# Performance work log

Hardware: AMD Instinct MI355X
Metric: run time of the kernel (lower is better)

## Reference

```python
import jax, jax.numpy as jnp
import numpy as np

DIAG = 64          # dynamic_mask_scale: |i-j| >= DIAG is masked
NEG_INF = float('-inf')

def _band_mask(L, diagonal):
    # True where masked out: j >= i + diagonal or i >= j + diagonal  <=>  |i-j| >= diagonal
    i = jnp.arange(L)[:, None]
    j = jnp.arange(L)[None, :]
    return jnp.abs(i - j) >= diagonal  # [L, L] bool

def setup_inputs() -> dict:
    key = jax.random.key(0)
    k1, k2, k3, k4 = jax.random.split(key, 4)
    B, L, H, E = 2, 2048, 8, 64
    queries = jax.random.normal(k1, (B, L, H, E), dtype=jnp.float32)
    keys = jax.random.normal(k2, (B, L, H, E), dtype=jnp.float32)
    values = jax.random.normal(k3, (B, L, H, E), dtype=jnp.float32)
    sigma = jax.random.normal(k4, (B, L, H), dtype=jnp.float32)
    attn_mask = jnp.zeros((B, 1, L, L), dtype=bool)  # unused (dynamic mask path)
    return {"queries": queries, "keys": keys, "values": values,
            "sigma": sigma, "attn_mask": attn_mask}

def reference(queries, keys, values, sigma, attn_mask):
    B, L, H, E = queries.shape
    scale = 1.0 / jnp.sqrt(jnp.float32(E))
    # scores: [B, H, L, S]
    scores = jnp.einsum('blhe,bshe->bhls', queries, keys)
    mask = _band_mask(L, DIAG)  # [L, L]
    scores = jnp.where(mask[None, None, :, :], NEG_INF, scores)
    attn = scale * scores
    series = jax.nn.softmax(attn, axis=-1)  # dropout p=0 -> identity
    V = jnp.einsum('bhls,bshd->blhd', series, values)
    return (V, series)
```

## Files before the change

### kernel.cpp

```cpp
#include <hip/hip_runtime.h>
#include <cstdint>

#define BB    2
#define LL    2048
#define HH    8
#define EE    64
#define DIAG  64
#define RR    16
#define WCAP  144
#define SK    68
#define PS    160
#define NT    256

__global__ __launch_bounds__(NT, 3) void anomaly_attn_kernel(
    const float* __restrict__ Q,
    const float* __restrict__ K,
    const float* __restrict__ V,
    float* __restrict__ outV,
    float* __restrict__ outS)
{
    __shared__ float lds_kv[WCAP * SK];
    __shared__ float lds_q[RR * EE];
    __shared__ float lds_sp[RR * PS];

    const int bid  = blockIdx.x;
    const int gblk = (bid & 7) * 256 + (bid >> 3);
    const int rb   = gblk & 127;
    const int h    = (gblk >> 7) & 7;
    const int b    = gblk >> 10;
    const int i0   = rb * RR;

    const int t    = threadIdx.x;
    const int wave = t >> 6;
    const int lane = t & 63;

    const size_t headOff = ((size_t)b * LL * HH + h) * EE;
    const int    rowStr  = HH * EE;

    const int j0 = i0 - (DIAG - 1);

    {
        const float4 z4 = make_float4(0.f, 0.f, 0.f, 0.f);
        float4* zp = (float4*)(lds_sp + wave * 4 * PS);
        for (int z = lane; z < 160; z += 64) zp[z] = z4;
    }

    {
        const int qrow = t >> 4, qf = t & 15;
        *(float4*)(lds_q + qrow * EE + qf * 4) =
            *(const float4*)(Q + headOff + (size_t)(i0 + qrow) * rowStr + qf * 4);
        for (int idx = t; idx < WCAP * 16; idx += NT) {
            const int trow = idx >> 4, tf = idx & 15;
            int j = j0 + trow; j = j < 0 ? 0 : (j > LL - 1 ? LL - 1 : j);
            *(float4*)(lds_kv + trow * SK + tf * 4) =
                *(const float4*)(K + headOff + (size_t)j * rowStr + tf * 4);
        }
    }
    __syncthreads();

    const float scale = 0.125f;
    for (int r4 = 0; r4 < 4; ++r4) {
        const int r = wave * 4 + r4;
        const int i = i0 + r;
        const float* qrow = lds_q + r * EE;
        const float* k1   = lds_kv + (r + lane) * SK;
        const float* k2   = k1 + 64 * SK;
        float s1 = 0.f, s2 = 0.f;
#pragma unroll
        for (int c = 0; c < 16; ++c) {
            const float4 q4 = *(const float4*)(qrow + c * 4);
            const float4 a4 = *(const float4*)(k1 + c * 4);
            const float4 b4 = *(const float4*)(k2 + c * 4);
            s1 += q4.x * a4.x + q4.y * a4.y + q4.z * a4.z + q4.w * a4.w;
            s2 += q4.x * b4.x + q4.y * b4.y + q4.z * b4.z + q4.w * b4.w;
        }
        const int  slot2 = lane + 64;
        const bool v1 = (i - (DIAG - 1) + lane) >= 0;
        const bool v2 = (slot2 < 2 * DIAG - 1) && (i - (DIAG - 1) + slot2 < LL);
        float sc1 = v1 ? s1 * scale : -3.0e38f;
        float sc2 = v2 ? s2 * scale : -3.0e38f;

        float m = fmaxf(sc1, sc2);
#pragma unroll
        for (int off = 1; off < 64; off <<= 1)
            m = fmaxf(m, __shfl_xor(m, off, 64));
        float p1 = v1 ? __expf(sc1 - m) : 0.f;
        float p2 = v2 ? __expf(sc2 - m) : 0.f;
        float l = p1 + p2;
#pragma unroll
        for (int off = 1; off < 64; off <<= 1)
            l += __shfl_xor(l, off, 64);
        const float inv = 1.0f / l;
        float* prow = lds_sp + r * PS;
        prow[16 + lane]      = p1 * inv;
        prow[80 + lane]      = p2 * inv;
    }
    __syncthreads();

    for (int idx = t; idx < WCAP * 16; idx += NT) {
        const int trow = idx >> 4, tf = idx & 15;
        int j = j0 + trow; j = j < 0 ? 0 : (j > LL - 1 ? LL - 1 : j);
        *(float4*)(lds_kv + trow * SK + tf * 4) =
            *(const float4*)(V + headOff + (size_t)j * rowStr + tf * 4);
    }
    __syncthreads();

    for (int r4 = 0; r4 < 4; ++r4) {
        const int r = wave * 4 + r4;
        const int i = i0 + r;
        float4* srow4 = (float4*)(outS + (((size_t)(b * HH + h)) * LL + i) * LL);
        const int start = i - (DIAG - 1);
        const float* sp = lds_sp + r * PS + 16;
#pragma unroll
        for (int k = 0; k < 8; ++k) {
            const int col4 = lane + k * 64;
            const int d0   = col4 * 4 - start;
            float4 v;
            int i0c = d0     < 0 ? 0 : (d0     > 127 ? 127 : d0);
            int i1c = d0 + 1 < 0 ? 0 : (d0 + 1 > 127 ? 127 : d0 + 1);
            int i2c = d0 + 2 < 0 ? 0 : (d0 + 2 > 127 ? 127 : d0 + 2);
            int i3c = d0 + 3 < 0 ? 0 : (d0 + 3 > 127 ? 127 : d0 + 3);
            v.x = (d0     >= 0) ? sp[i0c] : 0.f;
            v.y = (d0 + 1 >= 0) ? sp[i1c] : 0.f;
            v.z = (d0 + 2 >= 0) ? sp[i2c] : 0.f;
            v.w = (d0 + 3 >= 0) ? sp[i3c] : 0.f;
            srow4[col4] = v;
        }
    }

    {
        const int e4   = lane & 15;
        const int jsub = lane >> 4;
        const int rr0  = wave * 4;
        const float* pbase = lds_sp + rr0 * (PS - 1) + 16;
        float4 a0 = make_float4(0,0,0,0), a1 = a0, a2 = a0, a3 = a0;
#pragma unroll
        for (int k = 0; k < WCAP / 4; ++k) {
            const int jrel = jsub + 4 * k;
            const float4 vv = *(const float4*)(lds_kv + jrel * SK + e4 * 4);
            const float w0 = pbase[jrel];
            const float w1 = pbase[(PS - 1) + jrel];
            const float w2 = pbase[2 * (PS - 1) + jrel];
            const float w3 = pbase[3 * (PS - 1) + jrel];
            a0.x += w0 * vv.x; a0.y += w0 * vv.y; a0.z += w0 * vv.z; a0.w += w0 * vv.w;
            a1.x += w1 * vv.x; a1.y += w1 * vv.y; a1.z += w1 * vv.z; a1.w += w1 * vv.w;
            a2.x += w2 * vv.x; a2.y += w2 * vv.y; a2.z += w2 * vv.z; a2.w += w2 * vv.w;
            a3.x += w3 * vv.x; a3.y += w3 * vv.y; a3.z += w3 * vv.z; a3.w += w3 * vv.w;
        }
#pragma unroll
        for (int off = 16; off <= 32; off <<= 1) {
            a0.x += __shfl_xor(a0.x, off, 64); a0.y += __shfl_xor(a0.y, off, 64);
            a0.z += __shfl_xor(a0.z, off, 64); a0.w += __shfl_xor(a0.w, off, 64);
            a1.x += __shfl_xor(a1.x, off, 64); a1.y += __shfl_xor(a1.y, off, 64);
            a1.z += __shfl_xor(a1.z, off, 64); a1.w += __shfl_xor(a1.w, off, 64);
            a2.x += __shfl_xor(a2.x, off, 64); a2.y += __shfl_xor(a2.y, off, 64);
            a2.z += __shfl_xor(a2.z, off, 64); a2.w += __shfl_xor(a2.w, off, 64);
            a3.x += __shfl_xor(a3.x, off, 64); a3.y += __shfl_xor(a3.y, off, 64);
            a3.z += __shfl_xor(a3.z, off, 64); a3.w += __shfl_xor(a3.w, off, 64);
        }
        if (lane < 16) {
            float4* o0 = (float4*)(outV + headOff + (size_t)(i0 + rr0 + 0) * rowStr);
            float4* o1 = (float4*)(outV + headOff + (size_t)(i0 + rr0 + 1) * rowStr);
            float4* o2 = (float4*)(outV + headOff + (size_t)(i0 + rr0 + 2) * rowStr);
            float4* o3 = (float4*)(outV + headOff + (size_t)(i0 + rr0 + 3) * rowStr);
            o0[e4] = a0; o1[e4] = a1; o2[e4] = a2; o3[e4] = a3;
        }
    }
}

extern "C" void kernel_launch(void* const* d_in, const int* in_sizes, int n_in,
                              void* d_out, int out_size, void* d_ws, size_t ws_size,
                              hipStream_t stream) {
    const float* Q = (const float*)d_in[0];
    const float* K = (const float*)d_in[1];
    const float* V = (const float*)d_in[2];

    float* outV = (float*)d_out;
    float* outS = (float*)d_out + (size_t)BB * LL * HH * EE;

    const int grid = (BB * HH * LL) / RR;
    anomaly_attn_kernel<<<grid, NT, 0, stream>>>(Q, K, V, outV, outS);
}
```

Baseline: 344.2 us.

## Store probabilities in aligned window layout and pair rows in score computation

Switches the probability scratch layout from per-row diagonal offsets to a shared 4-aligned window starting at i0-64, so each score row can be written to global memory with aligned float4 LDS reads instead of four clamped scalar gathers. The QK score loop now processes two rows per iteration, sharing each K load between both rows. The reductions for the two rows are interleaved. The PV loop uses a plain stride. The kernel is dominated by the dense [L,L] score-matrix write, so the gain is mostly in instruction overhead around that store.

```diff
diff --git a/kernel.cpp b/kernel.cpp
--- a/kernel.cpp
+++ b/kernel.cpp
@@ -9,7 +9,7 @@
 #define RR    16
 #define WCAP  144
 #define SK    68
-#define PS    160
+#define PS    148
 #define NT    256
 
 __global__ __launch_bounds__(NT, 3) void anomaly_attn_kernel(
@@ -37,12 +37,13 @@
     const size_t headOff = ((size_t)b * LL * HH + h) * EE;
     const int    rowStr  = HH * EE;
 
-    const int j0 = i0 - (DIAG - 1);
+    const int j0  = i0 - 64;
+    const int j04 = j0 >> 2;
 
     {
         const float4 z4 = make_float4(0.f, 0.f, 0.f, 0.f);
         float4* zp = (float4*)(lds_sp + wave * 4 * PS);
-        for (int z = lane; z < 160; z += 64) zp[z] = z4;
+        for (int z = lane; z < PS; z += 64) zp[z] = z4;
     }
 
     {
@@ -59,41 +60,63 @@
     __syncthreads();
 
     const float scale = 0.125f;
-    for (int r4 = 0; r4 < 4; ++r4) {
-        const int r = wave * 4 + r4;
-        const int i = i0 + r;
-        const float* qrow = lds_q + r * EE;
-        const float* k1   = lds_kv + (r + lane) * SK;
-        const float* k2   = k1 + 64 * SK;
-        float s1 = 0.f, s2 = 0.f;
+#pragma unroll
+    for (int p = 0; p < 2; ++p) {
+        const int rA = wave * 4 + 2 * p;
+        const int rB = rA + 1;
+        const int jrelA = rA + 1 + lane;
+        const int jrelB = rA + 65 + lane;
+        const float* k1 = lds_kv + jrelA * SK;
+        const float* k2 = lds_kv + jrelB * SK;
+        const float* qA = lds_q + rA * EE;
+        const float* qB = lds_q + rB * EE;
+        float sA1 = 0.f, sA2 = 0.f, sB1 = 0.f, sB2 = 0.f;
 #pragma unroll
         for (int c = 0; c < 16; ++c) {
-            const float4 q4 = *(const float4*)(qrow + c * 4);
-            const float4 a4 = *(const float4*)(k1 + c * 4);
-            const float4 b4 = *(const float4*)(k2 + c * 4);
-            s1 += q4.x * a4.x + q4.y * a4.y + q4.z * a4.z + q4.w * a4.w;
-            s2 += q4.x * b4.x + q4.y * b4.y + q4.z * b4.z + q4.w * b4.w;
-        }
-        const int  slot2 = lane + 64;
-        const bool v1 = (i - (DIAG - 1) + lane) >= 0;
-        const bool v2 = (slot2 < 2 * DIAG - 1) && (i - (DIAG - 1) + slot2 < LL);
-        float sc1 = v1 ? s1 * scale : -3.0e38f;
-        float sc2 = v2 ? s2 * scale : -3.0e38f;
-
-        float m = fmaxf(sc1, sc2);
-#pragma unroll
-        for (int off = 1; off < 64; off <<= 1)
-            m = fmaxf(m, __shfl_xor(m, off, 64));
-        float p1 = v1 ? __expf(sc1 - m) : 0.f;
-        float p2 = v2 ? __expf(sc2 - m) : 0.f;
-        float l = p1 + p2;
-#pragma unroll
-        for (int off = 1; off < 64; off <<= 1)
-            l += __shfl_xor(l, off, 64);
-        const float inv = 1.0f / l;
-        float* prow = lds_sp + r * PS;
-        prow[16 + lane]      = p1 * inv;
-        prow[80 + lane]      = p2 * inv;
+            const float4 a4  = *(const float4*)(k1 + c * 4);
+            const float4 b4  = *(const float4*)(k2 + c * 4);
+            const float4 qa4 = *(const float4*)(qA + c * 4);
+            const float4 qb4 = *(const float4*)(qB + c * 4);
+            sA1 += qa4.x*a4.x + qa4.y*a4.y + qa4.z*a4.z + qa4.w*a4.w;
+            sA2 += qa4.x*b4.x + qa4.y*b4.y + qa4.z*b4.z + qa4.w*b4.w;
+            sB1 += qb4.x*a4.x + qb4.y*a4.y + qb4.z*a4.z + qb4.w*a4.w;
+            sB2 += qb4.x*b4.x + qb4.y*b4.y + qb4.z*b4.z + qb4.w*b4.w;
+        }
+        const int jA = j0 + jrelA;
+        const int jB = j0 + jrelB;
+        const bool vA1 = (jA >= 0);
+        const bool vA2 = (lane <= 62) && (jB < LL);
+        const bool vB1 = (lane >= 1) && (jA >= 0);
+        const bool vB2 = (jB < LL);
+        float eA1 = vA1 ? sA1 * scale : -3.0e38f;
+        float eA2 = vA2 ? sA2 * scale : -3.0e38f;
+        float eB1 = vB1 ? sB1 * scale : -3.0e38f;
+        float eB2 = vB2 ? sB2 * scale : -3.0e38f;
+
+        float mA = fmaxf(eA1, eA2);
+        float mB = fmaxf(eB1, eB2);
+#pragma unroll
+        for (int off = 1; off < 64; off <<= 1) {
+            mA = fmaxf(mA, __shfl_xor(mA, off, 64));
+            mB = fmaxf(mB, __shfl_xor(mB, off, 64));
+        }
+        float pA1 = vA1 ? __expf(eA1 - mA) : 0.f;
+        float pA2 = vA2 ? __expf(eA2 - mA) : 0.f;
+        float pB1 = vB1 ? __expf(eB1 - mB) : 0.f;
+        float pB2 = vB2 ? __expf(eB2 - mB) : 0.f;
+        float lA = pA1 + pA2;
+        float lB = pB1 + pB2;
+#pragma unroll
+        for (int off = 1; off < 64; off <<= 1) {
+            lA += __shfl_xor(lA, off, 64);
+            lB += __shfl_xor(lB, off, 64);
+        }
+        const float invA = 1.0f / lA;
+        const float invB = 1.0f / lB;
+        lds_sp[rA * PS + jrelA] = pA1 * invA;
+        lds_sp[rA * PS + jrelB] = pA2 * invA;
+        lds_sp[rB * PS + jrelA] = pB1 * invB;
+        lds_sp[rB * PS + jrelB] = pB2 * invB;
     }
     __syncthreads();
 
@@ -105,26 +128,22 @@
     }
     __syncthreads();
 
-    for (int r4 = 0; r4 < 4; ++r4) {
-        const int r = wave * 4 + r4;
-        const int i = i0 + r;
-        float4* srow4 = (float4*)(outS + (((size_t)(b * HH + h)) * LL + i) * LL);
-        const int start = i - (DIAG - 1);
-        const float* sp = lds_sp + r * PS + 16;
-#pragma unroll
-        for (int k = 0; k < 8; ++k) {
-            const int col4 = lane + k * 64;
-            const int d0   = col4 * 4 - start;
-            float4 v;
-            int i0c = d0     < 0 ? 0 : (d0     > 127 ? 127 : d0);
-            int i1c = d0 + 1 < 0 ? 0 : (d0 + 1 > 127 ? 127 : d0 + 1);
-            int i2c = d0 + 2 < 0 ? 0 : (d0 + 2 > 127 ? 127 : d0 + 2);
-            int i3c = d0 + 3 < 0 ? 0 : (d0 + 3 > 127 ? 127 : d0 + 3);
-            v.x = (d0     >= 0) ? sp[i0c] : 0.f;
-            v.y = (d0 + 1 >= 0) ? sp[i1c] : 0.f;
-            v.z = (d0 + 2 >= 0) ? sp[i2c] : 0.f;
-            v.w = (d0 + 3 >= 0) ? sp[i3c] : 0.f;
-            srow4[col4] = v;
+    {
+        const int wstart4 = j04 < 0 ? 0 : j04;
+        int wend4 = j04 + 36; if (wend4 > LL / 4) wend4 = LL / 4;
+        for (int r4 = 0; r4 < 4; ++r4) {
+            const int r = wave * 4 + r4;
+            const int i = i0 + r;
+            float4* srow4 = (float4*)(outS + (((size_t)(b * HH + h)) * LL + i) * LL);
+            const float4* sp4 = (const float4*)(lds_sp + r * PS);
+#pragma unroll
+            for (int k = 0; k < 8; ++k) {
+                const int col4 = lane + k * 64;
+                float4 v = make_float4(0.f, 0.f, 0.f, 0.f);
+                if (col4 >= wstart4 && col4 < wend4)
+                    v = sp4[col4 - j04];
+                srow4[col4] = v;
+            }
         }
     }
 
@@ -132,16 +151,16 @@
         const int e4   = lane & 15;
         const int jsub = lane >> 4;
         const int rr0  = wave * 4;
-        const float* pbase = lds_sp + rr0 * (PS - 1) + 16;
+        const float* pbase = lds_sp + rr0 * PS;
         float4 a0 = make_float4(0,0,0,0), a1 = a0, a2 = a0, a3 = a0;
 #pragma unroll
         for (int k = 0; k < WCAP / 4; ++k) {
             const int jrel = jsub + 4 * k;
             const float4 vv = *(const float4*)(lds_kv + jrel * SK + e4 * 4);
             const float w0 = pbase[jrel];
-            const float w1 = pbase[(PS - 1) + jrel];
-            const float w2 = pbase[2 * (PS - 1) + jrel];
-            const float w3 = pbase[3 * (PS - 1) + jrel];
+            const float w1 = pbase[PS + jrel];
+            const float w2 = pbase[2 * PS + jrel];
+            const float w3 = pbase[3 * PS + jrel];
             a0.x += w0 * vv.x; a0.y += w0 * vv.y; a0.z += w0 * vv.z; a0.w += w0 * vv.w;
             a1.x += w1 * vv.x; a1.y += w1 * vv.y; a1.z += w1 * vv.z; a1.w += w1 * vv.w;
             a2.x += w2 * vv.x; a2.y += w2 * vv.y; a2.z += w2 * vv.z; a2.w += w2 * vv.w;
```

Measured after the change: 336.0 us. 1.02x faster.
